# Optimization experiments

Measured on AMD Instinct MI355X. Metric: run time of the kernel, lower is better.

## Reference

```python
import jax, jax.numpy as jnp
import numpy as np

N_NODES = 50000


def setup_inputs() -> dict:
    key = jax.random.key(0)
    k1, k2, k3, k4, k5 = jax.random.split(key, 5)
    F_IN, F_OUT, E = 128, 128, 800000
    x = jax.random.normal(k1, (N_NODES, F_IN), dtype=jnp.float32)
    edge_index = jax.random.randint(k2, (2, E), 0, N_NODES, dtype=jnp.int64)
    # PyG Linear uses Kaiming-ish init; scale for stable magnitudes
    s = 1.0 / np.sqrt(F_IN)
    W_l = jax.random.normal(k3, (F_IN, F_OUT), dtype=jnp.float32) * s
    W_r = jax.random.normal(k4, (F_IN, F_OUT), dtype=jnp.float32) * s
    b = jax.random.normal(k5, (F_OUT,), dtype=jnp.float32) * s
    return {"x": x, "edge_index": edge_index, "W_l": W_l, "W_r": W_r, "b": b}


def reference(x, edge_index, W_l, W_r, b):
    # SAGEConv (mean aggr): out = mean_{j in N(i)} x_j @ W_l + x_i @ W_r + b
    src, dst = edge_index[0], edge_index[1]
    msgs = x[src]  # [E, F_in] gather
    summed = jax.ops.segment_sum(msgs, dst, num_segments=N_NODES)  # [N, F_in]
    deg = jax.ops.segment_sum(jnp.ones_like(dst, dtype=x.dtype), dst,
                              num_segments=N_NODES)  # [N]
    mean = summed / jnp.maximum(deg, 1.0)[:, None]
    return mean @ W_l + x @ W_r + b
```

## Files before the change

kernel.cpp:

```cpp
#include <hip/hip_runtime.h>

#define N_NODES 50000
#define F 128
#define NBIN 98
#define BIN_NODES 512
#define BINCAP 10000
#define NB_A 256
#define NB_CV 6250
#define NB_BT 128

typedef __attribute__((ext_vector_type(8))) short bf16x8;
typedef __attribute__((ext_vector_type(4))) float f32x4;
typedef __attribute__((ext_vector_type(4))) unsigned int u32x4;

__device__ __forceinline__ unsigned short f2bf(float f) {
    unsigned u = __float_as_uint(f);
    unsigned r = u + 0x7FFFu + ((u >> 16) & 1u);
    return (unsigned short)(r >> 16);
}

__global__ __launch_bounds__(128) void init_kernel(int* __restrict__ cursor)
{
    const int t = threadIdx.x;
    if (t < NBIN) cursor[t] = t * BINCAP;
}

__global__ __launch_bounds__(256) void fused_prep_kernel(
    const float* __restrict__ x, unsigned short* __restrict__ xb,
    const int* __restrict__ src, const int* __restrict__ dst,
    int* __restrict__ cursor, unsigned* __restrict__ binbuf,
    const float* __restrict__ Wl, const float* __restrict__ Wr,
    unsigned short* __restrict__ Bt, int E)
{
    const int bid = blockIdx.x;
    const int t = threadIdx.x;

    if (bid < NB_A) {
        __shared__ int hist[NBIN], hist2[NBIN], base[NBIN];
        if (t < NBIN) { hist[t] = 0; hist2[t] = 0; }
        __syncthreads();

        const int e0 = bid * 3125;
        for (int j = t; j < 3125; j += 256)
            atomicAdd(&hist[dst[e0 + j] >> 9], 1);
        __syncthreads();

        if (t < NBIN) base[t] = atomicAdd(&cursor[t], hist[t]);
        __syncthreads();

        for (int j = t; j < 3125; j += 256) {
            const int d = dst[e0 + j];
            const int s = src[e0 + j];
            const int b = d >> 9;
            const int r = atomicAdd(&hist2[b], 1);
            binbuf[base[b] + r] = (unsigned)s | ((unsigned)(d & 511) << 16);
        }
    } else if (bid < NB_A + NB_CV) {
        const int i = (bid - NB_A) * 256 + t;
        const float4 v = reinterpret_cast<const float4*>(x)[i];
        ushort4 o;
        o.x = f2bf(v.x); o.y = f2bf(v.y); o.z = f2bf(v.z); o.w = f2bf(v.w);
        reinterpret_cast<ushort4*>(xb)[i] = o;
    } else {
        const int gid = (bid - NB_A - NB_CV) * 256 + t;
        const int n = gid >> 8;
        const int k = gid & 255;
        const float v = (k < F) ? Wl[k * F + n] : Wr[(k - F) * F + n];
        Bt[gid] = f2bf(v);
    }
}

__global__ __launch_bounds__(512) void binscatter_kernel(
    const unsigned* __restrict__ binbuf, const int* __restrict__ cursor,
    unsigned short* __restrict__ csr, int* __restrict__ start,
    int* __restrict__ deg)
{
    __shared__ int degL[BIN_NODES], lofs[BIN_NODES], cnt2[BIN_NODES];
    __shared__ unsigned short lbc[BINCAP];
    __shared__ int wsumS[8];
    __shared__ int pre[128];
    __shared__ int cbaseS;

    const int b = blockIdx.x, t = threadIdx.x;
    const int lane = t & 63, wid = t >> 6;

    degL[t] = 0; cnt2[t] = 0;
    if (t < 128) {
        int v = (t < NBIN) ? (cursor[t] - t * BINCAP) : 0;
        int incl = v;
#pragma unroll
        for (int off = 1; off < 64; off <<= 1) {
            const int u = __shfl_up(incl, off, 64);
            if (lane >= off) incl += u;
        }
        pre[t] = incl;
    }
    __syncthreads();
    if (t == 0)
        cbaseS = (b == 0) ? 0 : ((b <= 64) ? pre[b - 1]
                                           : pre[63] + pre[b - 1]);
    const int lo = b * BINCAP;
    const int hi = cursor[b];
    const int n = hi - lo;

    for (int j = lo + t; j < hi; j += 512)
        atomicAdd(&degL[binbuf[j] >> 16], 1);
    __syncthreads();

    {
        const int v = degL[t];
        int incl = v;
#pragma unroll
        for (int off = 1; off < 64; off <<= 1) {
            const int u = __shfl_up(incl, off, 64);
            if (lane >= off) incl += u;
        }
        if (lane == 63) wsumS[wid] = incl;
        __syncthreads();
        if (t == 0) {
            int run = 0;
#pragma unroll
            for (int w = 0; w < 8; ++w) { const int s = wsumS[w]; wsumS[w] = run; run += s; }
        }
        __syncthreads();
        lofs[t] = wsumS[wid] + incl - v;
    }
    __syncthreads();

    for (int j = lo + t; j < hi; j += 512) {
        const unsigned p = binbuf[j];
        const int dl = p >> 16;
        const int r = atomicAdd(&cnt2[dl], 1);
        lbc[lofs[dl] + r] = (unsigned short)(p & 0xFFFFu);
    }
    __syncthreads();

    const int gn0 = b * BIN_NODES;
    if (gn0 + t < N_NODES) {
        start[gn0 + t] = cbaseS + lofs[t];
        deg[gn0 + t] = degL[t];
    }
    for (int i = t; i < n; i += 512) csr[cbaseS + i] = lbc[i];
}

__global__ __launch_bounds__(256) void agg_out_kernel(
    const unsigned short* __restrict__ xb,
    const unsigned short* __restrict__ csr,
    const int* __restrict__ start,
    const int* __restrict__ deg,
    const unsigned short* __restrict__ Bt,
    const float* __restrict__ bias,
    float* __restrict__ out)
{
    __shared__ __align__(16) unsigned short mean_s[16][136];
    __shared__ float cs[16][132];

    const int t = threadIdx.x;
    const int w = t >> 6, lane = t & 63;
    const int li = lane & 15, g = lane >> 4;
    const int mbase = blockIdx.x * 16;
    const int colu = 2 * lane;

#define ACC2(v)                                    \
    {                                              \
        a0 += __uint_as_float((v) << 16);          \
        a1 += __uint_as_float((v) & 0xFFFF0000u);  \
    }

    for (int q = 0; q < 4; ++q) {
        const int ln = w * 4 + q;
        const int node = mbase + ln;
        const int s0 = start[node];
        const int d = deg[node];

        const int idx = (lane < d) ? (int)csr[s0 + lane] : 0;

        float a0 = 0.f, a1 = 0.f;
        for (int j = 0; j < d; j += 8) {
            const int r0 = __shfl(idx, j + 0);
            const int r1 = __shfl(idx, j + 1);
            const int r2 = __shfl(idx, j + 2);
            const int r3 = __shfl(idx, j + 3);
            const int r4 = __shfl(idx, j + 4);
            const int r5 = __shfl(idx, j + 5);
            const int r6 = __shfl(idx, j + 6);
            const int r7 = __shfl(idx, j + 7);
            const unsigned v0 = *reinterpret_cast<const unsigned*>(&xb[(size_t)r0 * F + colu]);
            const unsigned v1 = *reinterpret_cast<const unsigned*>(&xb[(size_t)r1 * F + colu]);
            const unsigned v2 = *reinterpret_cast<const unsigned*>(&xb[(size_t)r2 * F + colu]);
            const unsigned v3 = *reinterpret_cast<const unsigned*>(&xb[(size_t)r3 * F + colu]);
            const unsigned v4 = *reinterpret_cast<const unsigned*>(&xb[(size_t)r4 * F + colu]);
            const unsigned v5 = *reinterpret_cast<const unsigned*>(&xb[(size_t)r5 * F + colu]);
            const unsigned v6 = *reinterpret_cast<const unsigned*>(&xb[(size_t)r6 * F + colu]);
            const unsigned v7 = *reinterpret_cast<const unsigned*>(&xb[(size_t)r7 * F + colu]);
            const int rem = d - j;
            ACC2(v0)
            if (rem > 1) ACC2(v1)
            if (rem > 2) ACC2(v2)
            if (rem > 3) ACC2(v3)
            if (rem > 4) ACC2(v4)
            if (rem > 5) ACC2(v5)
            if (rem > 6) ACC2(v6)
            if (rem > 7) ACC2(v7)
        }

        const float inv = (d > 0) ? (1.0f / (float)d) : 1.0f;
        const unsigned u =
            (unsigned)f2bf(a0 * inv) | ((unsigned)f2bf(a1 * inv) << 16);
        *reinterpret_cast<unsigned*>(&mean_s[ln][colu]) = u;
    }
#undef ACC2
    __syncthreads();

    const int arow = mbase + li;
    const int kchunk = g * 8;

    bf16x8 a[8];
#pragma unroll
    for (int s = 0; s < 4; ++s) {
        a[s] = *reinterpret_cast<const bf16x8*>(&mean_s[li][s * 32 + kchunk]);
        a[s + 4] = *reinterpret_cast<const bf16x8*>(
            &xb[(size_t)arow * F + s * 32 + kchunk]);
    }

    f32x4 acc[2];
    acc[0] = (f32x4){0.f, 0.f, 0.f, 0.f};
    acc[1] = (f32x4){0.f, 0.f, 0.f, 0.f};

#pragma unroll
    for (int s = 0; s < 8; ++s) {
#pragma unroll
        for (int nt = 0; nt < 2; ++nt) {
            const bf16x8 bf = *reinterpret_cast<const bf16x8*>(
                &Bt[(size_t)((w * 2 + nt) * 16 + li) * 256 + s * 32 + kchunk]);
            acc[nt] = __builtin_amdgcn_mfma_f32_16x16x32_bf16(a[s], bf, acc[nt], 0, 0, 0);
        }
    }

#pragma unroll
    for (int nt = 0; nt < 2; ++nt) {
        const int col = (w * 2 + nt) * 16 + li;
        const float bv = bias[col];
#pragma unroll
        for (int r = 0; r < 4; ++r)
            cs[g * 4 + r][col] = acc[nt][r] + bv;
    }
    __syncthreads();

#pragma unroll
    for (int i = 0; i < 2; ++i) {
        const int idx = t + i * 256;
        const int r = idx >> 5;
        const int c4 = (idx & 31) << 2;
        float4 v;
        v.x = cs[r][c4 + 0];
        v.y = cs[r][c4 + 1];
        v.z = cs[r][c4 + 2];
        v.w = cs[r][c4 + 3];
        *reinterpret_cast<float4*>(&out[(size_t)(mbase + r) * F + c4]) = v;
    }
}

extern "C" void kernel_launch(void* const* d_in, const int* in_sizes, int n_in,
                              void* d_out, int out_size, void* d_ws, size_t ws_size,
                              hipStream_t stream)
{
    const float* x  = (const float*)d_in[0];
    const int*   ei = (const int*)d_in[1];
    const float* Wl = (const float*)d_in[2];
    const float* Wr = (const float*)d_in[3];
    const float* b  = (const float*)d_in[4];
    float* out = (float*)d_out;

    const int E = in_sizes[1] / 2;
    const int* src = ei;
    const int* dst = ei + E;

    int* cursor = (int*)d_ws;
    int* start  = cursor + 128;
    int* deg    = start + 50176;
    unsigned* binbuf = (unsigned*)(deg + 50176);
    unsigned short* csr = (unsigned short*)(binbuf + 980000);
    unsigned short* xb  = csr + 800064;
    unsigned short* Bt  = xb + (size_t)N_NODES * F;

    init_kernel<<<1, 128, 0, stream>>>(cursor);

    fused_prep_kernel<<<NB_A + NB_CV + NB_BT, 256, 0, stream>>>(
        x, xb, src, dst, cursor, binbuf, Wl, Wr, Bt, E);

    binscatter_kernel<<<NBIN, 512, 0, stream>>>(binbuf, cursor, csr, start, deg);

    agg_out_kernel<<<N_NODES / 16, 256, 0, stream>>>(
        xb, csr, start, deg, Bt, b, out);
}
```

Measured before the change: 97.27 us.

## Gather four nodes per wave with 16-byte loads and double-buffered prefetch

The mean-aggregation gather is restructured. Each wave now splits into four 16-lane groups, one per destination node, so the wave's four nodes are gathered at the same time instead of one after another. Each lane loads 8 bf16 values (16 bytes) per neighbor row instead of 2. Neighbor rows are loaded in blocks of 8, and two register buffers alternate so the next block's loads are in flight while the current block is accumulated. The goal is more memory-level parallelism and fewer, wider load instructions in this latency-bound gather, at the cost of more registers per thread.

```diff
diff --git a/kernel.cpp b/kernel.cpp
--- a/kernel.cpp
+++ b/kernel.cpp
@@ -157,59 +157,107 @@
 
     const int t = threadIdx.x;
     const int w = t >> 6, lane = t & 63;
-    const int li = lane & 15, g = lane >> 4;
+    const int g = lane >> 4, li = lane & 15;
+    const int ln = w * 4 + g;
     const int mbase = blockIdx.x * 16;
-    const int colu = 2 * lane;
-
-#define ACC2(v)                                    \
-    {                                              \
-        a0 += __uint_as_float((v) << 16);          \
-        a1 += __uint_as_float((v) & 0xFFFF0000u);  \
-    }
-
-    for (int q = 0; q < 4; ++q) {
-        const int ln = w * 4 + q;
-        const int node = mbase + ln;
-        const int s0 = start[node];
-        const int d = deg[node];
-
-        const int idx = (lane < d) ? (int)csr[s0 + lane] : 0;
-
-        float a0 = 0.f, a1 = 0.f;
-        for (int j = 0; j < d; j += 8) {
-            const int r0 = __shfl(idx, j + 0);
-            const int r1 = __shfl(idx, j + 1);
-            const int r2 = __shfl(idx, j + 2);
-            const int r3 = __shfl(idx, j + 3);
-            const int r4 = __shfl(idx, j + 4);
-            const int r5 = __shfl(idx, j + 5);
-            const int r6 = __shfl(idx, j + 6);
-            const int r7 = __shfl(idx, j + 7);
-            const unsigned v0 = *reinterpret_cast<const unsigned*>(&xb[(size_t)r0 * F + colu]);
-            const unsigned v1 = *reinterpret_cast<const unsigned*>(&xb[(size_t)r1 * F + colu]);
-            const unsigned v2 = *reinterpret_cast<const unsigned*>(&xb[(size_t)r2 * F + colu]);
-            const unsigned v3 = *reinterpret_cast<const unsigned*>(&xb[(size_t)r3 * F + colu]);
-            const unsigned v4 = *reinterpret_cast<const unsigned*>(&xb[(size_t)r4 * F + colu]);
-            const unsigned v5 = *reinterpret_cast<const unsigned*>(&xb[(size_t)r5 * F + colu]);
-            const unsigned v6 = *reinterpret_cast<const unsigned*>(&xb[(size_t)r6 * F + colu]);
-            const unsigned v7 = *reinterpret_cast<const unsigned*>(&xb[(size_t)r7 * F + colu]);
-            const int rem = d - j;
-            ACC2(v0)
-            if (rem > 1) ACC2(v1)
-            if (rem > 2) ACC2(v2)
-            if (rem > 3) ACC2(v3)
-            if (rem > 4) ACC2(v4)
-            if (rem > 5) ACC2(v5)
-            if (rem > 6) ACC2(v6)
-            if (rem > 7) ACC2(v7)
-        }
-
-        const float inv = (d > 0) ? (1.0f / (float)d) : 1.0f;
-        const unsigned u =
-            (unsigned)f2bf(a0 * inv) | ((unsigned)f2bf(a1 * inv) << 16);
-        *reinterpret_cast<unsigned*>(&mean_s[ln][colu]) = u;
-    }
-#undef ACC2
+    const int node = mbase + ln;
+
+    const int cnt_total = deg[node];
+    const int s0 = start[node];
+
+    float a0 = 0.f, a1 = 0.f, a2 = 0.f, a3 = 0.f;
+    float a4 = 0.f, a5 = 0.f, a6 = 0.f, a7 = 0.f;
+
+    const int colu = li * 8;
+    const int gbase = g * 16;
+
+    const int idx0 = (li      < cnt_total) ? (int)csr[s0 + li]      : 0;
+    const int idx1 = (li + 16 < cnt_total) ? (int)csr[s0 + li + 16] : 0;
+    const int idx2 = (li + 32 < cnt_total) ? (int)csr[s0 + li + 32] : 0;
+    const int idx3 = (li + 48 < cnt_total) ? (int)csr[s0 + li + 48] : 0;
+
+    u32x4 A0, A1, A2, A3, A4, A5, A6, A7;
+    u32x4 B0, B1, B2, B3, B4, B5, B6, B7;
+
+#define ISSUE(R0, R1, R2, R3, R4, R5, R6, R7, b)                            \
+    {                                                                       \
+        const int c_ = (b) >> 1;                                            \
+        int sel_ = idx0;                                                    \
+        sel_ = (c_ == 1) ? idx1 : sel_;                                     \
+        sel_ = (c_ == 2) ? idx2 : sel_;                                     \
+        sel_ = (c_ == 3) ? idx3 : sel_;                                     \
+        const int o_ = gbase + (((b) & 1) << 3);                            \
+        const int r0_ = __shfl(sel_, o_ + 0);                               \
+        const int r1_ = __shfl(sel_, o_ + 1);                               \
+        const int r2_ = __shfl(sel_, o_ + 2);                               \
+        const int r3_ = __shfl(sel_, o_ + 3);                               \
+        const int r4_ = __shfl(sel_, o_ + 4);                               \
+        const int r5_ = __shfl(sel_, o_ + 5);                               \
+        const int r6_ = __shfl(sel_, o_ + 6);                               \
+        const int r7_ = __shfl(sel_, o_ + 7);                               \
+        R0 = *reinterpret_cast<const u32x4*>(&xb[(size_t)r0_ * F + colu]);  \
+        R1 = *reinterpret_cast<const u32x4*>(&xb[(size_t)r1_ * F + colu]);  \
+        R2 = *reinterpret_cast<const u32x4*>(&xb[(size_t)r2_ * F + colu]);  \
+        R3 = *reinterpret_cast<const u32x4*>(&xb[(size_t)r3_ * F + colu]);  \
+        R4 = *reinterpret_cast<const u32x4*>(&xb[(size_t)r4_ * F + colu]);  \
+        R5 = *reinterpret_cast<const u32x4*>(&xb[(size_t)r5_ * F + colu]);  \
+        R6 = *reinterpret_cast<const u32x4*>(&xb[(size_t)r6_ * F + colu]);  \
+        R7 = *reinterpret_cast<const u32x4*>(&xb[(size_t)r7_ * F + colu]);  \
+    }
+
+#define ACCV(v)                                     \
+    {                                               \
+        a0 += __uint_as_float((v).x << 16);         \
+        a1 += __uint_as_float((v).x & 0xFFFF0000u); \
+        a2 += __uint_as_float((v).y << 16);         \
+        a3 += __uint_as_float((v).y & 0xFFFF0000u); \
+        a4 += __uint_as_float((v).z << 16);         \
+        a5 += __uint_as_float((v).z & 0xFFFF0000u); \
+        a6 += __uint_as_float((v).w << 16);         \
+        a7 += __uint_as_float((v).w & 0xFFFF0000u); \
+    }
+
+#define CONSUME(R0, R1, R2, R3, R4, R5, R6, R7, b)  \
+    {                                               \
+        const int rem_ = cnt_total - (b) * 8;       \
+        ACCV(R0)                                    \
+        if (rem_ > 1) ACCV(R1)                      \
+        if (rem_ > 2) ACCV(R2)                      \
+        if (rem_ > 3) ACCV(R3)                      \
+        if (rem_ > 4) ACCV(R4)                      \
+        if (rem_ > 5) ACCV(R5)                      \
+        if (rem_ > 6) ACCV(R6)                      \
+        if (rem_ > 7) ACCV(R7)                      \
+    }
+
+    const int nb = (cnt_total + 7) >> 3;
+
+    if (nb > 0) {
+        ISSUE(A0, A1, A2, A3, A4, A5, A6, A7, 0)
+        if (nb > 1) ISSUE(B0, B1, B2, B3, B4, B5, B6, B7, 1)
+
+        for (int b = 0; b < nb; b += 2) {
+            CONSUME(A0, A1, A2, A3, A4, A5, A6, A7, b)
+            if (b + 2 < nb) ISSUE(A0, A1, A2, A3, A4, A5, A6, A7, b + 2)
+            if (b + 1 < nb) {
+                CONSUME(B0, B1, B2, B3, B4, B5, B6, B7, b + 1)
+                if (b + 3 < nb) ISSUE(B0, B1, B2, B3, B4, B5, B6, B7, b + 3)
+            }
+        }
+    }
+#undef ISSUE
+#undef ACCV
+#undef CONSUME
+
+    {
+        const float inv = (cnt_total > 0) ? (1.0f / (float)cnt_total) : 1.0f;
+        u32x4 u;
+        u.x = (unsigned)f2bf(a0 * inv) | ((unsigned)f2bf(a1 * inv) << 16);
+        u.y = (unsigned)f2bf(a2 * inv) | ((unsigned)f2bf(a3 * inv) << 16);
+        u.z = (unsigned)f2bf(a4 * inv) | ((unsigned)f2bf(a5 * inv) << 16);
+        u.w = (unsigned)f2bf(a6 * inv) | ((unsigned)f2bf(a7 * inv) << 16);
+        *reinterpret_cast<u32x4*>(&mean_s[ln][colu]) = u;
+    }
     __syncthreads();
 
     const int arow = mbase + li;
```

Result: faster. 87.48 us (-10.1%).
